# Kernel tuning notes

Hardware: AMD Instinct MI355X
Metric: run time of the kernel (lower is better)

The kernel has to match this reference:

```python
import jax, jax.numpy as jnp
import numpy as np

B, N, DIM_IN, DIM_INNER, DIM_OUT = 4, 4096, 512, 512, 512
SCALE = DIM_INNER ** -0.5


def setup_inputs() -> dict:
    key = jax.random.key(0)
    k1, k2, k3, k4, k5 = jax.random.split(key, 5)
    x = jax.random.normal(k1, (B, N, DIM_IN), dtype=jnp.float32)
    prev = jax.random.normal(k2, (B, N, N), dtype=jnp.float32)
    # nn.Linear(dim_in, 3*dim_inner, bias=False): store as [dim_in, 3*dim_inner] for x @ W
    Wqkv = jax.random.normal(k3, (DIM_IN, 3 * DIM_INNER), dtype=jnp.float32) * (DIM_IN ** -0.5)
    Wout = jax.random.normal(k4, (DIM_INNER, DIM_OUT), dtype=jnp.float32) * (DIM_INNER ** -0.5)
    bout = jax.random.normal(k5, (DIM_OUT,), dtype=jnp.float32) * 0.01
    return {"x": x, "prev": prev, "Wqkv": Wqkv, "Wout": Wout, "bout": bout}


def reference(x, prev, Wqkv, Wout, bout):
    # qkv projection and split
    qkv = x @ Wqkv                                   # [b, n, 3*d]
    q, k, v = jnp.split(qkv, 3, axis=-1)             # each [b, n, d]
    sim = jnp.einsum('bid,bjd->bij', q, k) * SCALE   # [b, n, n]
    sim = sim + prev                                  # additive previous-score bias
    # causal mask: strict upper triangle filled with -finfo.max (matches torch masked_fill_)
    n = sim.shape[-1]
    causal_mask = jnp.triu(jnp.ones((n, n), dtype=bool), k=1)
    neg_max = jnp.asarray(-jnp.finfo(q.dtype).max, dtype=sim.dtype)
    sim = jnp.where(causal_mask[None, :, :], neg_max, sim)
    attn = jax.nn.softmax(sim, axis=-1)              # [b, n, n]
    out = jnp.einsum('bij,bjd->bid', attn, v)        # [b, n, d]
    out = out @ Wout + bout                          # [b, n, dim_out]
    return (out, sim)
```

## Files before the change

### kernel.cpp

```cpp
#include <hip/hip_runtime.h>
#include <float.h>
#include <math.h>

#define B_    4
#define N_    4096
#define DIN   512
#define DI    512
#define DOUTD 512
#define DQKV  1536
#define MTOT  (B_*N_)

static constexpr float kScale  = 0.044194173824159216f;
static constexpr float kNegMax = -3.0e38f;

typedef float     f32x4 __attribute__((ext_vector_type(4)));
typedef short     bf16x8 __attribute__((ext_vector_type(8)));
typedef _Float16  f16x4 __attribute__((ext_vector_type(4)));
typedef _Float16  f16x8 __attribute__((ext_vector_type(8)));

__device__ __forceinline__ unsigned short f2b(float f) {
    unsigned u = __builtin_bit_cast(unsigned, f);
    unsigned r = (u + 0x7fffu + ((u >> 16) & 1u)) >> 16;
    return (unsigned short)r;
}

__device__ __forceinline__ void ldreg_b16(bf16x8 v[4], const short* src,
                                          int srcStride, int k0)
{
    int t = threadIdx.x;
    int r = t >> 1, h = t & 1;
    const short* p = src + (size_t)r * srcStride + k0 + h * 32;
    #pragma unroll
    for (int q = 0; q < 4; ++q) v[q] = *reinterpret_cast<const bf16x8*>(p + q * 8);
}

__device__ __forceinline__ void streg_b16(short* lds, const bf16x8 v[4])
{
    int t = threadIdx.x;
    int r = t >> 1, h = t & 1;
    #pragma unroll
    for (int q = 0; q < 4; ++q) {
        int slot = (h * 4 + q) ^ (r & 7);
        *reinterpret_cast<bf16x8*>(&lds[r * 64 + slot * 8]) = v[q];
    }
}

__device__ __forceinline__ void ldreg_f32(f32x4 v[8], const float* src,
                                          int srcStride, int k0)
{
    int t = threadIdx.x;
    int r = t >> 1, h = t & 1;
    const float* p = src + (size_t)r * srcStride + k0 + h * 32;
    #pragma unroll
    for (int q = 0; q < 8; ++q) v[q] = *reinterpret_cast<const f32x4*>(p + q * 4);
}

__device__ __forceinline__ void streg_f32(short* lds, const f32x4 v[8])
{
    int t = threadIdx.x;
    int r = t >> 1, h = t & 1;
    #pragma unroll
    for (int q = 0; q < 4; ++q) {
        bf16x8 w;
        w[0] = (short)f2b(v[2 * q][0]); w[1] = (short)f2b(v[2 * q][1]);
        w[2] = (short)f2b(v[2 * q][2]); w[3] = (short)f2b(v[2 * q][3]);
        w[4] = (short)f2b(v[2 * q + 1][0]); w[5] = (short)f2b(v[2 * q + 1][1]);
        w[6] = (short)f2b(v[2 * q + 1][2]); w[7] = (short)f2b(v[2 * q + 1][3]);
        int slot = (h * 4 + q) ^ (r & 7);
        *reinterpret_cast<bf16x8*>(&lds[r * 64 + slot * 8]) = w;
    }
}

__device__ __forceinline__ bf16x8 ld_frag(const short* lds, int rowbase, int kk)
{
    int l = threadIdx.x & 63;
    int r = rowbase + (l & 15);
    int slot = (kk * 4 + (l >> 4)) ^ (r & 7);
    return *reinterpret_cast<const bf16x8*>(&lds[r * 64 + slot * 8]);
}

__global__ __launch_bounds__(256)
void cvt_wt(const float* __restrict__ W, short* __restrict__ Wt, int K, int N)
{
    __shared__ float t[64][65];
    const int n0 = blockIdx.x * 64, k0 = blockIdx.y * 64;
    const int tid = threadIdx.x;
    #pragma unroll
    for (int q = 0; q < 4; ++q) {
        int r = (tid >> 4) + q * 16, c4 = (tid & 15) * 4;
        float4 f = *reinterpret_cast<const float4*>(&W[(size_t)(k0 + r) * N + n0 + c4]);
        t[r][c4] = f.x; t[r][c4 + 1] = f.y; t[r][c4 + 2] = f.z; t[r][c4 + 3] = f.w;
    }
    __syncthreads();
    #pragma unroll
    for (int p = 0; p < 2; ++p) {
        int s = tid * 2 + p;
        int n = s >> 3, k8 = (s & 7) * 8;
        bf16x8 v;
        #pragma unroll
        for (int e = 0; e < 8; ++e) v[e] = (short)f2b(t[k8 + e][n]);
        *reinterpret_cast<bf16x8*>(&Wt[(size_t)(n0 + n) * K + k0 + k8]) = v;
    }
}

template<bool AF32, bool OUTF32, bool BIAS, bool VFUSE>
__global__ __launch_bounds__(256)
void gemm_mfma(const void* __restrict__ Ap, const short* __restrict__ Bt,
               const float* __restrict__ bias, void* __restrict__ Cp,
               short* __restrict__ Vt, int Nld, int K)
{
    const int bm = blockIdx.y * 128;
    const int bn = blockIdx.x * 128;
    __shared__ short smem[2 * 128 * 64];
    short* As = smem;
    short* Bs = smem + 128 * 64;
    const int tid = threadIdx.x, lane = tid & 63, wid = tid >> 6;
    const int wr = (wid >> 1) * 64, wc = (wid & 1) * 64;
    f32x4 acc[4][4] = {};

    const float* Af = (const float*)Ap + (size_t)bm * K;
    const short* Ab = (const short*)Ap + (size_t)bm * K;
    const short* Bb = Bt + (size_t)bn * K;

    bf16x8 av[4]; f32x4 af[8]; bf16x8 bv[4];
    if (AF32) ldreg_f32(af, Af, K, 0); else ldreg_b16(av, Ab, K, 0);
    ldreg_b16(bv, Bb, K, 0);

    for (int k0 = 0; k0 < K; k0 += 64) {
        if (AF32) streg_f32(As, af); else streg_b16(As, av);
        streg_b16(Bs, bv);
        __syncthreads();
        if (k0 + 64 < K) {
            if (AF32) ldreg_f32(af, Af, K, k0 + 64); else ldreg_b16(av, Ab, K, k0 + 64);
            ldreg_b16(bv, Bb, K, k0 + 64);
        }
        __builtin_amdgcn_s_setprio(1);
        #pragma unroll
        for (int kk = 0; kk < 2; ++kk) {
            bf16x8 a[4], bb[4];
            #pragma unroll
            for (int m = 0; m < 4; ++m) a[m] = ld_frag(As, wr + m * 16, kk);
            #pragma unroll
            for (int n = 0; n < 4; ++n) bb[n] = ld_frag(Bs, wc + n * 16, kk);
            #pragma unroll
            for (int m = 0; m < 4; ++m)
                #pragma unroll
                for (int n = 0; n < 4; ++n)
                    acc[m][n] = __builtin_amdgcn_mfma_f32_16x16x32_bf16(bb[n], a[m], acc[m][n], 0, 0, 0);
        }
        __builtin_amdgcn_s_setprio(0);
        __syncthreads();
    }

    if (VFUSE && bn >= 1024) {
        short* Ct = smem;
        #pragma unroll
        for (int m = 0; m < 4; ++m) {
            const int rl = wr + m * 16 + (lane & 15);
            #pragma unroll
            for (int n = 0; n < 4; ++n) {
                const int cl = wc + n * 16 + (lane >> 4) * 4;
                short4 o;
                o.x = (short)f2b(acc[m][n][0]); o.y = (short)f2b(acc[m][n][1]);
                o.z = (short)f2b(acc[m][n][2]); o.w = (short)f2b(acc[m][n][3]);
                *reinterpret_cast<short4*>(&Ct[rl * 128 + cl]) = o;
            }
        }
        __syncthreads();
        const int b = bm >> 12, n0 = bm & 4095, d0 = bn - 1024;
        const int d = tid >> 1, h = tid & 1;
        short* dst = Vt + (size_t)b * DI * N_ + (size_t)(d0 + d) * N_ + n0 + h * 64;
        #pragma unroll
        for (int q = 0; q < 8; ++q) {
            bf16x8 v;
            #pragma unroll
            for (int e = 0; e < 8; ++e) v[e] = Ct[(h * 64 + q * 8 + e) * 128 + d];
            *reinterpret_cast<bf16x8*>(&dst[q * 8]) = v;
        }
        return;
    }

    const int rb = bm + wr + (lane & 15);
    const int cb = bn + wc + (lane >> 4) * 4;
    #pragma unroll
    for (int m = 0; m < 4; ++m) {
        const int row = rb + m * 16;
        #pragma unroll
        for (int n = 0; n < 4; ++n) {
            const int colb = cb + n * 16;
            f32x4 v = acc[m][n];
            if (BIAS) {
                f32x4 bi = *reinterpret_cast<const f32x4*>(&bias[colb]);
                v += bi;
            }
            if (OUTF32) {
                *reinterpret_cast<f32x4*>(&((float*)Cp)[(size_t)row * Nld + colb]) = v;
            } else {
                short4 o;
                o.x = (short)f2b(v[0]); o.y = (short)f2b(v[1]);
                o.z = (short)f2b(v[2]); o.w = (short)f2b(v[3]);
                *reinterpret_cast<short4*>(&((short*)Cp)[(size_t)row * Nld + colb]) = o;
            }
        }
    }
}

__global__ __launch_bounds__(256)
void sim_mfma(const short* __restrict__ qkvb, const float* __restrict__ prev,
              _Float16* __restrict__ simh, float* __restrict__ Pm, float* __restrict__ Pl)
{
    const int x = blockIdx.x;
    const int g = (x & 7) * 264 + (x >> 3);
    const int b = g / 528;
    const int t = g - b * 528;
    int iT = (int)((sqrtf(8.0f * (float)t + 1.0f) - 1.0f) * 0.5f);
    while ((iT + 1) * (iT + 2) / 2 <= t) ++iT;
    while (iT * (iT + 1) / 2 > t) --iT;
    const int jT = t - iT * (iT + 1) / 2;
    const int i0 = iT * 128;
    const int j0 = jT * 128;
    const int tid = threadIdx.x;

    _Float16* simb = simh + (size_t)b * N_ * N_;
    __shared__ short Qs[128 * 64];
    __shared__ short Ks[128 * 64];
    __shared__ float wm[2][128], wl[2][128];
    const short* qb = qkvb + (size_t)(b * N_ + i0) * DQKV;
    const short* kb = qkvb + (size_t)(b * N_ + j0) * DQKV + DI;
    const int lane = tid & 63, wid = tid >> 6;
    const int wr = (wid >> 1) * 64, wc = (wid & 1) * 64;
    f32x4 acc[4][4] = {};

    bf16x8 qv[4], kv[4];
    ldreg_b16(qv, qb, DQKV, 0);
    ldreg_b16(kv, kb, DQKV, 0);

    for (int k0 = 0; k0 < DI; k0 += 64) {
        streg_b16(Qs, qv);
        streg_b16(Ks, kv);
        __syncthreads();
        if (k0 + 64 < DI) {
            ldreg_b16(qv, qb, DQKV, k0 + 64);
            ldreg_b16(kv, kb, DQKV, k0 + 64);
        }
        __builtin_amdgcn_s_setprio(1);
        #pragma unroll
        for (int kk = 0; kk < 2; ++kk) {
            bf16x8 a[4], bb[4];
            #pragma unroll
            for (int m = 0; m < 4; ++m) a[m] = ld_frag(Qs, wr + m * 16, kk);
            #pragma unroll
            for (int n = 0; n < 4; ++n) bb[n] = ld_frag(Ks, wc + n * 16, kk);
            #pragma unroll
            for (int m = 0; m < 4; ++m)
                #pragma unroll
                for (int n = 0; n < 4; ++n)
                    acc[m][n] = __builtin_amdgcn_mfma_f32_16x16x32_bf16(bb[n], a[m], acc[m][n], 0, 0, 0);
        }
        __builtin_amdgcn_s_setprio(0);
        __syncthreads();
    }
    const float* prevb = prev + (size_t)b * N_ * N_;
    const int ib = i0 + wr + (lane & 15);
    const int jb = j0 + wc + (lane >> 4) * 4;
    const int wcIdx = wid & 1;
    #pragma unroll
    for (int m = 0; m < 4; ++m) {
        const int row = ib + m * 16;
        float mx = -FLT_MAX;
        f32x4 ovals[4];
        #pragma unroll
        for (int n = 0; n < 4; ++n) {
            const int colb = jb + n * 16;
            f32x4 p = *reinterpret_cast<const f32x4*>(&prevb[(size_t)row * N_ + colb]);
            f32x4 o;
            f16x4 oh;
            #pragma unroll
            for (int reg = 0; reg < 4; ++reg) {
                o[reg] = (colb + reg <= row) ? fmaf(acc[m][n][reg], kScale, p[reg]) : kNegMax;
                oh[reg] = (_Float16)o[reg];
            }
            *reinterpret_cast<f16x4*>(&simb[(size_t)row * N_ + colb]) = oh;
            ovals[n] = o;
            #pragma unroll
            for (int reg = 0; reg < 4; ++reg) mx = fmaxf(mx, o[reg]);
        }
        mx = fmaxf(mx, __shfl_xor(mx, 16));
        mx = fmaxf(mx, __shfl_xor(mx, 32));
        float s = 0.f;
        #pragma unroll
        for (int n = 0; n < 4; ++n)
            #pragma unroll
            for (int reg = 0; reg < 4; ++reg) s += __expf(ovals[n][reg] - mx);
        s += __shfl_xor(s, 16);
        s += __shfl_xor(s, 32);
        if ((lane >> 4) == 0) {
            int rr = wr + m * 16 + (lane & 15);
            wm[wcIdx][rr] = mx;
            wl[wcIdx][rr] = s;
        }
    }
    __syncthreads();
    if (tid < 128) {
        float m0 = wm[0][tid], m1 = wm[1][tid];
        float l0 = wl[0][tid], l1 = wl[1][tid];
        float M, L;
        if (m1 <= -1.0e38f) { M = m0; L = l0; }
        else {
            M = fmaxf(m0, m1);
            L = l0 * __expf(m0 - M) + l1 * __expf(m1 - M);
        }
        size_t slot = ((size_t)b * 32 + jT) * N_ + i0 + tid;
        Pm[slot] = M;
        Pl[slot] = L;
    }
}

__global__ __launch_bounds__(256)
void attn_v2(const _Float16* __restrict__ simh, const short* __restrict__ Vt,
             const float* __restrict__ Pm, const float* __restrict__ Pl,
             short* __restrict__ out0b)
{
    const int x = blockIdx.x;
    const int g = ((x & 7) + ((x >> 4) << 3)) * 2 + ((x >> 3) & 1);
    const int iT = 63 - (g >> 3);
    const int b = (g >> 1) & 3, dchunk = g & 1;
    const int i0 = iT * 64, d0 = dchunk * 256;
    const int tid = threadIdx.x;
    const int lane = tid & 63, wid = tid >> 6;
    const int wd = wid * 64;

    __shared__ short Ps[64 * 64];
    __shared__ short Vs[256 * 64];
    __shared__ float rm[64], ri[64];
    if (tid < 64) {
        const int i = i0 + tid;
        const int nt = (i >> 7) + 1;
        const float* pm = Pm + (size_t)b * 32 * N_ + i;
        const float* pl = Pl + (size_t)b * 32 * N_ + i;
        float M = -FLT_MAX;
        for (int u = 0; u < nt; ++u) M = fmaxf(M, pm[(size_t)u * N_]);
        float L = 0.f;
        for (int u = 0; u < nt; ++u) L += pl[(size_t)u * N_] * __expf(pm[(size_t)u * N_] - M);
        rm[tid] = M;
        ri[tid] = 1.0f / L;
    }
    __syncthreads();

    const _Float16* simb = simh + (size_t)b * N_ * N_ + (size_t)i0 * N_;
    const short* vtb  = Vt + (size_t)b * DI * N_ + (size_t)d0 * N_;
    const int pr = tid >> 2, pc = (tid & 3) * 16;
    const int vr = tid >> 3, vc = (tid & 7) * 8;
    const int vslot = ((tid & 7) ^ (vr & 7)) * 8;
    const float pmr = rm[pr], pir = ri[pr];
    f32x4 acc[4][4] = {};
    const int nk = iT + 1;

    f16x8 hvA[2]; bf16x8 vvA[8];
    {
        const _Float16* p = simb + (size_t)pr * N_ + pc;
        hvA[0] = *reinterpret_cast<const f16x8*>(p);
        hvA[1] = *reinterpret_cast<const f16x8*>(p + 8);
        #pragma unroll
        for (int q = 0; q < 8; ++q)
            vvA[q] = *reinterpret_cast<const bf16x8*>(vtb + (size_t)(vr + q * 32) * N_ + vc);
    }
    for (int kt = 0; kt < nk; ++kt) {
        f16x8 hvB[2]; bf16x8 vvB[8];
        const bool more = (kt + 1 < nk);
        if (more) {
            const _Float16* p = simb + (size_t)pr * N_ + (kt + 1) * 64 + pc;
            hvB[0] = *reinterpret_cast<const f16x8*>(p);
            hvB[1] = *reinterpret_cast<const f16x8*>(p + 8);
            #pragma unroll
            for (int q = 0; q < 8; ++q)
                vvB[q] = *reinterpret_cast<const bf16x8*>(
                    vtb + (size_t)(vr + q * 32) * N_ + (kt + 1) * 64 + vc);
        }
        bf16x8 w0, w1;
        #pragma unroll
        for (int e = 0; e < 8; ++e) {
            w0[e] = (short)f2b(__expf((float)hvA[0][e] - pmr) * pir);
            w1[e] = (short)f2b(__expf((float)hvA[1][e] - pmr) * pir);
        }
        {
            int sb = (tid & 3) * 2;
            *reinterpret_cast<bf16x8*>(&Ps[pr * 64 + ((sb    ) ^ (pr & 7)) * 8]) = w0;
            *reinterpret_cast<bf16x8*>(&Ps[pr * 64 + ((sb + 1) ^ (pr & 7)) * 8]) = w1;
        }
        #pragma unroll
        for (int q = 0; q < 8; ++q)
            *reinterpret_cast<bf16x8*>(&Vs[(vr + q * 32) * 64 + vslot]) = vvA[q];
        __syncthreads();
        #pragma unroll
        for (int kk = 0; kk < 2; ++kk) {
            bf16x8 a[4], bb[4];
            #pragma unroll
            for (int m = 0; m < 4; ++m) a[m] = ld_frag(Ps, m * 16, kk);
            #pragma unroll
            for (int n = 0; n < 4; ++n) bb[n] = ld_frag(Vs, wd + n * 16, kk);
            #pragma unroll
            for (int m = 0; m < 4; ++m)
                #pragma unroll
                for (int n = 0; n < 4; ++n)
                    acc[m][n] = __builtin_amdgcn_mfma_f32_16x16x32_bf16(bb[n], a[m], acc[m][n], 0, 0, 0);
        }
        __syncthreads();
        if (more) {
            hvA[0] = hvB[0]; hvA[1] = hvB[1];
            #pragma unroll
            for (int q = 0; q < 8; ++q) vvA[q] = vvB[q];
        }
    }
    #pragma unroll
    for (int m = 0; m < 4; ++m) {
        const int i = i0 + m * 16 + (lane & 15);
        #pragma unroll
        for (int n = 0; n < 4; ++n) {
            const int db = d0 + wd + n * 16 + (lane >> 4) * 4;
            short4 o;
            o.x = (short)f2b(acc[m][n][0]);
            o.y = (short)f2b(acc[m][n][1]);
            o.z = (short)f2b(acc[m][n][2]);
            o.w = (short)f2b(acc[m][n][3]);
            *reinterpret_cast<short4*>(&out0b[(size_t)(b * N_ + i) * DI + db]) = o;
        }
    }
}

extern "C" void kernel_launch(void* const* d_in, const int* in_sizes, int n_in,
                              void* d_out, int out_size, void* d_ws, size_t ws_size,
                              hipStream_t stream)
{
    (void)in_sizes; (void)n_in; (void)out_size; (void)ws_size;
    const float* x    = (const float*)d_in[0];
    const float* prev = (const float*)d_in[1];
    const float* Wqkv = (const float*)d_in[2];
    const float* Wout = (const float*)d_in[3];
    const float* bout = (const float*)d_in[4];

    float* out = (float*)d_out;
    _Float16* simh = (_Float16*)(out + (size_t)MTOT * DOUTD);

    short* qkvb   = (short*)d_ws;
    short* out0b  = qkvb + (size_t)MTOT * DQKV;
    short* Vt     = out0b + (size_t)MTOT * DI;
    short* Wqkvt  = Vt + (size_t)MTOT * DI;
    short* Woutt  = Wqkvt + (size_t)DQKV * DIN;
    float* Pm     = (float*)(Woutt + (size_t)DI * DOUTD);
    float* Pl     = Pm + (size_t)B_ * 32 * N_;

    cvt_wt<<<dim3(DQKV / 64, DIN / 64), 256, 0, stream>>>(Wqkv, Wqkvt, DIN, DQKV);
    cvt_wt<<<dim3(DOUTD / 64, DI / 64), 256, 0, stream>>>(Wout, Woutt, DI, DOUTD);

    gemm_mfma<true, false, false, true><<<dim3(DQKV / 128, MTOT / 128), 256, 0, stream>>>(
        x, Wqkvt, nullptr, qkvb, Vt, DQKV, DIN);

    sim_mfma<<<dim3(528 * B_), 256, 0, stream>>>(qkvb, prev, simh, Pm, Pl);

    attn_v2<<<dim3(512), 256, 0, stream>>>(simh, Vt, Pm, Pl, out0b);

    gemm_mfma<false, true, true, false><<<dim3(DOUTD / 128, MTOT / 128), 256, 0, stream>>>(
        out0b, Woutt, bout, out, nullptr, DOUTD, DI);
}
```

Before: 291.7 us.

## Merge weight-convert launches, prefetch prev rows, and coalesce sim loads in attn

The two weight-conversion launches become a single 256-block kernel that picks its matrix by block index, saving one launch. In the sim epilogue, the prev tile for the next 16-row group is loaded before the current group is processed, so global load latency overlaps the softmax stats work. In attn_v2, each thread now reads 8 contiguous fp16 sim values from two rows 32 apart instead of 16 from one row. This gives more coalesced global reads and a simpler LDS write pattern, at the cost of extra registers for the prefetched data.

```diff
diff --git a/kernel.cpp b/kernel.cpp
--- a/kernel.cpp
+++ b/kernel.cpp
@@ -80,10 +80,14 @@
 }
 
 __global__ __launch_bounds__(256)
-void cvt_wt(const float* __restrict__ W, short* __restrict__ Wt, int K, int N)
-{
+void cvt_wt2(const float* __restrict__ Wqkv, short* __restrict__ Wqkvt,
+             const float* __restrict__ Wout, short* __restrict__ Woutt)
+{
+    const float* W; short* Wt; int K, N, n0, k0;
+    int bz = blockIdx.x;
+    if (bz < 192) { W = Wqkv; Wt = Wqkvt; K = DIN; N = DQKV; n0 = (bz % 24) * 64; k0 = (bz / 24) * 64; }
+    else { bz -= 192; W = Wout; Wt = Woutt; K = DI; N = DOUTD; n0 = (bz & 7) * 64; k0 = (bz >> 3) * 64; }
     __shared__ float t[64][65];
-    const int n0 = blockIdx.x * 64, k0 = blockIdx.y * 64;
     const int tid = threadIdx.x;
     #pragma unroll
     for (int q = 0; q < 4; ++q) {
@@ -264,20 +268,32 @@
     const int ib = i0 + wr + (lane & 15);
     const int jb = j0 + wc + (lane >> 4) * 4;
     const int wcIdx = wid & 1;
+
+    f32x4 pv[4];
+    #pragma unroll
+    for (int n = 0; n < 4; ++n)
+        pv[n] = *reinterpret_cast<const f32x4*>(&prevb[(size_t)ib * N_ + (jb + n * 16)]);
+
     #pragma unroll
     for (int m = 0; m < 4; ++m) {
         const int row = ib + m * 16;
+        f32x4 pnx[4];
+        if (m < 3) {
+            #pragma unroll
+            for (int n = 0; n < 4; ++n)
+                pnx[n] = *reinterpret_cast<const f32x4*>(
+                    &prevb[(size_t)(row + 16) * N_ + (jb + n * 16)]);
+        }
         float mx = -FLT_MAX;
         f32x4 ovals[4];
         #pragma unroll
         for (int n = 0; n < 4; ++n) {
             const int colb = jb + n * 16;
-            f32x4 p = *reinterpret_cast<const f32x4*>(&prevb[(size_t)row * N_ + colb]);
             f32x4 o;
             f16x4 oh;
             #pragma unroll
             for (int reg = 0; reg < 4; ++reg) {
-                o[reg] = (colb + reg <= row) ? fmaf(acc[m][n][reg], kScale, p[reg]) : kNegMax;
+                o[reg] = (colb + reg <= row) ? fmaf(acc[m][n][reg], kScale, pv[n][reg]) : kNegMax;
                 oh[reg] = (_Float16)o[reg];
             }
             *reinterpret_cast<f16x4*>(&simb[(size_t)row * N_ + colb]) = oh;
@@ -298,6 +314,10 @@
             int rr = wr + m * 16 + (lane & 15);
             wm[wcIdx][rr] = mx;
             wl[wcIdx][rr] = s;
+        }
+        if (m < 3) {
+            #pragma unroll
+            for (int n = 0; n < 4; ++n) pv[n] = pnx[n];
         }
     }
     __syncthreads();
@@ -349,18 +369,19 @@
 
     const _Float16* simb = simh + (size_t)b * N_ * N_ + (size_t)i0 * N_;
     const short* vtb  = Vt + (size_t)b * DI * N_ + (size_t)d0 * N_;
-    const int pr = tid >> 2, pc = (tid & 3) * 16;
+    const int r0 = tid >> 3, c8 = tid & 7;
+    const int slot0 = (c8 ^ (r0 & 7)) * 8;
+    const float pm0 = rm[r0],      pi0 = ri[r0];
+    const float pm1 = rm[r0 + 32], pi1 = ri[r0 + 32];
     const int vr = tid >> 3, vc = (tid & 7) * 8;
     const int vslot = ((tid & 7) ^ (vr & 7)) * 8;
-    const float pmr = rm[pr], pir = ri[pr];
     f32x4 acc[4][4] = {};
     const int nk = iT + 1;
 
     f16x8 hvA[2]; bf16x8 vvA[8];
     {
-        const _Float16* p = simb + (size_t)pr * N_ + pc;
-        hvA[0] = *reinterpret_cast<const f16x8*>(p);
-        hvA[1] = *reinterpret_cast<const f16x8*>(p + 8);
+        hvA[0] = *reinterpret_cast<const f16x8*>(simb + (size_t)r0 * N_ + c8 * 8);
+        hvA[1] = *reinterpret_cast<const f16x8*>(simb + (size_t)(r0 + 32) * N_ + c8 * 8);
         #pragma unroll
         for (int q = 0; q < 8; ++q)
             vvA[q] = *reinterpret_cast<const bf16x8*>(vtb + (size_t)(vr + q * 32) * N_ + vc);
@@ -369,9 +390,8 @@
         f16x8 hvB[2]; bf16x8 vvB[8];
         const bool more = (kt + 1 < nk);
         if (more) {
-            const _Float16* p = simb + (size_t)pr * N_ + (kt + 1) * 64 + pc;
-            hvB[0] = *reinterpret_cast<const f16x8*>(p);
-            hvB[1] = *reinterpret_cast<const f16x8*>(p + 8);
+            hvB[0] = *reinterpret_cast<const f16x8*>(simb + (size_t)r0 * N_ + (kt + 1) * 64 + c8 * 8);
+            hvB[1] = *reinterpret_cast<const f16x8*>(simb + (size_t)(r0 + 32) * N_ + (kt + 1) * 64 + c8 * 8);
             #pragma unroll
             for (int q = 0; q < 8; ++q)
                 vvB[q] = *reinterpret_cast<const bf16x8*>(
@@ -380,14 +400,11 @@
         bf16x8 w0, w1;
         #pragma unroll
         for (int e = 0; e < 8; ++e) {
-            w0[e] = (short)f2b(__expf((float)hvA[0][e] - pmr) * pir);
-            w1[e] = (short)f2b(__expf((float)hvA[1][e] - pmr) * pir);
-        }
-        {
-            int sb = (tid & 3) * 2;
-            *reinterpret_cast<bf16x8*>(&Ps[pr * 64 + ((sb    ) ^ (pr & 7)) * 8]) = w0;
-            *reinterpret_cast<bf16x8*>(&Ps[pr * 64 + ((sb + 1) ^ (pr & 7)) * 8]) = w1;
-        }
+            w0[e] = (short)f2b(__expf((float)hvA[0][e] - pm0) * pi0);
+            w1[e] = (short)f2b(__expf((float)hvA[1][e] - pm1) * pi1);
+        }
+        *reinterpret_cast<bf16x8*>(&Ps[r0 * 64 + slot0]) = w0;
+        *reinterpret_cast<bf16x8*>(&Ps[(r0 + 32) * 64 + slot0]) = w1;
         #pragma unroll
         for (int q = 0; q < 8; ++q)
             *reinterpret_cast<bf16x8*>(&Vs[(vr + q * 32) * 64 + vslot]) = vvA[q];
@@ -450,8 +467,7 @@
     float* Pm     = (float*)(Woutt + (size_t)DI * DOUTD);
     float* Pl     = Pm + (size_t)B_ * 32 * N_;
 
-    cvt_wt<<<dim3(DQKV / 64, DIN / 64), 256, 0, stream>>>(Wqkv, Wqkvt, DIN, DQKV);
-    cvt_wt<<<dim3(DOUTD / 64, DI / 64), 256, 0, stream>>>(Wout, Woutt, DI, DOUTD);
+    cvt_wt2<<<dim3(256), 256, 0, stream>>>(Wqkv, Wqkvt, Wout, Woutt);
 
     gemm_mfma<true, false, false, true><<<dim3(DQKV / 128, MTOT / 128), 256, 0, stream>>>(
         x, Wqkvt, nullptr, qkvb, Vt, DQKV, DIN);
```

Measured after the change: 288.1 us. No clear change (-1.2%).
